# Kernel optimization log

Hardware: AMD Instinct MI355X
Metric: run time of the kernel (lower is better)

## Reference

```python
import jax, jax.numpy as jnp
import numpy as np

# CE module constants (from init_kwargs / chosen input shape)
K = 7        # ksize
S1 = 4       # stride_1 (query patches / fold stride)
S2 = 1       # stride_2 (key/value patches)
SCALE = 10.0 # softmax_scale
C_IN = 32    # in_channels
IC = 4       # inter_channels
B, H, W = 2, 128, 128
PAD1 = ((1, 2), (1, 2))  # 'same' padding for k=7, stride=4, H=W=128 (top=1,bot=2)
PAD2 = ((3, 3), (3, 3))  # 'same' padding for k=7, stride=1


def _conv(x, w, b, stride, pad):
    y = jax.lax.conv_general_dilated(x, w, (stride, stride), pad,
                                     dimension_numbers=('NCHW', 'OIHW', 'NCHW'))
    return y + b[None, :, None, None]


def _patches(x, k, stride, pad):
    # returns [B, L, C*k*k] with feature order (C, kh, kw) == torch.nn.Unfold
    p = jax.lax.conv_general_dilated_patches(x, (k, k), (stride, stride), padding=pad)
    bb, f, ho, wo = p.shape
    return p.reshape(bb, f, ho * wo).transpose(0, 2, 1), ho, wo


def _fold_norm(out, ic, k, hh, ww, stride, pad, lh, lw):
    # out: [B, L1, ic*k*k] -> F.fold(..., (hh,ww), k, padding=pad, stride=stride),
    # normalized by overlap count fold(unfold(ones)).
    bb = out.shape[0]
    z = out.reshape(bb, lh, lw, ic, k, k).transpose(0, 3, 1, 2, 4, 5)  # [B,ic,lh,lw,k,k]
    hp, wp = hh + 2 * pad, ww + 2 * pad
    acc = jnp.zeros((bb, ic, hp, wp), out.dtype)
    cnt = jnp.zeros((hp, wp), out.dtype)
    ih = jnp.arange(lh) * stride
    iw = jnp.arange(lw) * stride
    one = jnp.ones((lh, lw), out.dtype)
    for ki in range(k):
        for kj in range(k):
            r = (ih + ki)[:, None]
            c = (iw + kj)[None, :]
            acc = acc.at[:, :, r, c].add(z[:, :, :, :, ki, kj])
            cnt = cnt.at[r, c].add(one)
    acc = acc[:, :, pad:pad + hh, pad:pad + ww]
    cnt = cnt[pad:pad + hh, pad:pad + ww]
    return acc / cnt


def setup_inputs() -> dict:
    key = jax.random.key(0)
    ks = jax.random.split(key, 13)
    f = K * K * IC  # 196
    g = f // 4      # 49
    s = 0.05
    return {
        'b':       jax.random.normal(ks[0], (B, C_IN, H, W), jnp.float32),
        'w_g':     (jax.random.normal(ks[1], (IC, C_IN, 3, 3), jnp.float32) * s),
        'b_g':     jnp.zeros((IC,), jnp.float32),
        'w_theta': (jax.random.normal(ks[2], (IC, C_IN, 1, 1), jnp.float32) * s),
        'b_theta': jnp.zeros((IC,), jnp.float32),
        'w_fc1':   (jax.random.normal(ks[3], (g, f), jnp.float32) * s),
        'b_fc1':   jnp.zeros((g,), jnp.float32),
        'w_fc2':   (jax.random.normal(ks[4], (g, f), jnp.float32) * s),
        'b_fc2':   jnp.zeros((g,), jnp.float32),
        'w_thr':   (jax.random.normal(ks[5], (1, C_IN, K, K), jnp.float32) * s),
        'b_thr':   jnp.zeros((1,), jnp.float32),
        'w_bias':  (jax.random.normal(ks[6], (1, C_IN, K, K), jnp.float32) * s),
        'b_bias':  jnp.zeros((1,), jnp.float32),
    }


def reference(b, w_g, b_g, w_theta, b_theta, w_fc1, b_fc1, w_fc2, b_fc2,
              w_thr, b_thr, w_bias, b_bias):
    bb = b.shape[0]
    b1 = _conv(b, w_g, b_g, 1, ((1, 1), (1, 1)))        # g: 3x3, pad 1 -> [B,IC,H,W]
    b2 = _conv(b, w_theta, b_theta, 1, ((0, 0), (0, 0)))  # theta: 1x1
    # adaptive threshold / bias per coarse patch (conv on same-padded b)
    thr = _conv(b, w_thr, b_thr, S1, PAD1).reshape(bb, -1)    # [B, L1]
    bias = _conv(b, w_bias, b_bias, S1, PAD1).reshape(bb, -1)  # [B, L1]
    p28, lh, lw = _patches(b1, K, S1, PAD1)   # queries  [B, L1, IC*49]
    p112, _, _ = _patches(b2, K, S2, PAD2)    # values   [B, L2, IC*49]
    p112_2, _, _ = _patches(b1, K, S2, PAD2)  # keys     [B, L2, IC*49] (b3 = b1)
    wi = jax.nn.relu(jnp.einsum('blf,gf->blg', p28, w_fc1) + b_fc1)     # [B,L1,49]
    xi = jax.nn.relu(jnp.einsum('blf,gf->blg', p112_2, w_fc2) + b_fc2)  # [B,L2,49]
    score = jnp.einsum('bpg,bqg->bpq', wi, xi)  # [B, L1, L2]
    mask = jax.nn.relu(score - score.mean(-1, keepdims=True) * thr[:, :, None]
                       + bias[:, :, None])
    mask_b = (mask != 0.0).astype(score.dtype)
    attn = jax.nn.softmax(score * mask * SCALE, axis=-1) * mask_b
    out = jnp.einsum('bpq,bqf->bpf', attn, p112)  # [B, L1, IC*49]
    return _fold_norm(out, IC, K, H, W, S1, 3, lh, lw)  # [B, IC, H, W]
```

## Files before the change

### kernel.cpp

```cpp
#include <hip/hip_runtime.h>
#include <hip/hip_fp16.h>
#include <math.h>

static constexpr int C_IN = 32, IC = 4, H = 128, W = 128, G = 49, F = 196;
static constexpr int L = 1024, Q = 16384;
static constexpr float SCALE = 10.f;
static constexpr int NH = 8;
static constexpr int B2P_PER_B = 8*5*136*136;

typedef __attribute__((ext_vector_type(8))) short short8;
typedef __attribute__((ext_vector_type(4))) float floatx4;

__device__ __forceinline__ unsigned short f2bf(float f){
  unsigned u = __float_as_uint(f);
  return (unsigned short)((u + 0x7fffu + ((u >> 16) & 1u)) >> 16);
}
__device__ __forceinline__ float bf2f(unsigned short h){
  return __uint_as_float(((unsigned)h) << 16);
}
__device__ __forceinline__ floatx4 mfma16(uint4 a, uint4 b, floatx4 c){
  return __builtin_amdgcn_mfma_f32_16x16x32_bf16(*(short8*)&a, *(short8*)&b, c, 0, 0, 0);
}

__global__ __launch_bounds__(256) void k_front(
    const float* __restrict__ bsrc, const float* __restrict__ w_g, const float* __restrict__ b_g,
    const float* __restrict__ w_t, const float* __restrict__ b_t,
    float* __restrict__ b1, unsigned short* __restrict__ b2p) {
  __shared__ float s_wg[IC*C_IN*9];
  __shared__ float s_wt[IC*C_IN];
  __shared__ float s_bg[IC], s_bt[IC];
  for (int i = threadIdx.x; i < IC*C_IN*9; i += 256) s_wg[i] = w_g[i];
  for (int i = threadIdx.x; i < IC*C_IN; i += 256) s_wt[i] = w_t[i];
  if (threadIdx.x < IC) { s_bg[threadIdx.x] = b_g[threadIdx.x]; s_bt[threadIdx.x] = b_t[threadIdx.x]; }
  __syncthreads();
  int idx = blockIdx.x*256 + threadIdx.x;
  int x = idx & 127, y = (idx>>7) & 127, bb = idx >> 14;
  const float* bp = bsrc + (size_t)bb*C_IN*H*W;
  float a1[IC], a2[IC];
  #pragma unroll
  for (int o=0;o<IC;o++){ a1[o]=s_bg[o]; a2[o]=s_bt[o]; }
  for (int c=0;c<C_IN;c++){
    const float* bc = bp + c*H*W;
    float ctr = bc[y*W+x];
    #pragma unroll
    for (int o=0;o<IC;o++) a2[o] += ctr * s_wt[o*C_IN + c];
    #pragma unroll
    for (int dy=0; dy<3; dy++){
      int yy = y + dy - 1;
      if ((unsigned)yy >= (unsigned)H) continue;
      #pragma unroll
      for (int dx=0; dx<3; dx++){
        int xx = x + dx - 1;
        if ((unsigned)xx >= (unsigned)W) continue;
        float v = bc[yy*W+xx];
        #pragma unroll
        for (int o=0;o<IC;o++) a1[o] += v * s_wg[(o*C_IN + c)*9 + dy*3 + dx];
      }
    }
  }
  unsigned short* bp2 = b2p + (size_t)bb*B2P_PER_B;
  #pragma unroll
  for (int o=0;o<IC;o++){
    b1[((size_t)(bb*IC+o)*H + y)*W + x] = a1[o];
    unsigned short h = f2bf(a2[o]);
    #pragma unroll
    for (int s=0;s<7;s++){
      int u = x + 3 - s;
      if (u >= 0)
        bp2[((s*5 + o)*136 + (y+3))*136 + u] = h;
    }
  }
}

__global__ __launch_bounds__(128) void k_xi(
    const float* __restrict__ b1, const float* __restrict__ w_fc2, const float* __restrict__ b_fc2,
    unsigned short* __restrict__ xiT, float* __restrict__ meanxi) {
  __shared__ float s_wT[196][16];
  __shared__ float s_p[IC*7*136];
  __shared__ float s_red[2][16];
  int tid = threadIdx.x;
  int blk = blockIdx.x;
  int gq = blk & 3, y = (blk >> 2) & 127, bb = blk >> 9;
  int g0 = (gq == 0) ? 0 : (13 + 12*(gq-1));
  int ng = (gq == 0) ? 13 : 12;
  for (int i = tid; i < 196*16; i += 128){
    int f = i >> 4, gi = i & 15;
    s_wT[f][gi] = (gi < ng) ? w_fc2[(size_t)(g0+gi)*196 + f] : 0.f;
  }
  for (int i=tid; i<IC*7*136; i+=128) {
    int col = i % 136; int t = i / 136; int ki = t % 7; int c = t / 7;
    int gy = y - 3 + ki, gx = col - 3;
    float v = 0.f;
    if ((unsigned)gy < (unsigned)H && (unsigned)gx < (unsigned)W && col < 134)
      v = b1[((size_t)(bb*IC+c)*H + gy)*W + gx];
    s_p[i] = v;
  }
  __syncthreads();
  int x = tid;
  float acc[13];
  #pragma unroll
  for (int ai=0; ai<13; ++ai) acc[ai] = (ai < ng) ? b_fc2[g0+ai] : 0.f;
  for (int c=0;c<IC;c++)
    for (int ki=0;ki<7;ki++){
      const float* prow = &s_p[(c*7+ki)*136 + x];
      #pragma unroll
      for (int kj=0;kj<7;kj++){
        float pv = prow[kj];
        int f = c*49 + ki*7 + kj;
        const float4* wr = (const float4*)&s_wT[f][0];
        float4 w0 = wr[0], w1 = wr[1], w2 = wr[2], w3 = wr[3];
        float wv[16] = {w0.x,w0.y,w0.z,w0.w, w1.x,w1.y,w1.z,w1.w,
                        w2.x,w2.y,w2.z,w2.w, w3.x,w3.y,w3.z,w3.w};
        #pragma unroll
        for (int ai=0; ai<13; ++ai) acc[ai] += pv * wv[ai];
      }
    }
  #pragma unroll
  for (int ai=0; ai<13; ++ai) acc[ai] = fmaxf(acc[ai], 0.f);
  #pragma unroll
  for (int ai=0; ai<13; ++ai){
    if (ai >= ng) break;
    float v = acc[ai];
    #pragma unroll
    for (int off=1; off<64; off<<=1) v += __shfl_xor(v, off);
    if ((tid&63)==0) s_red[tid>>6][ai] = v;
  }
  __syncthreads();
  if (tid < ng) atomicAdd(&meanxi[bb*G + g0 + tid], (s_red[0][tid]+s_red[1][tid]) * (1.f/(float)Q));
  unsigned short* xr = xiT + ((size_t)((bb<<14) + y*W + x))*128;
  #pragma unroll
  for (int ai=0; ai<13; ++ai){
    if (ai >= ng) break;
    float w = acc[ai];
    unsigned short h = f2bf(w);
    float l = w - bf2f(h);
    xr[g0+ai] = h;
    xr[64+g0+ai] = f2bf(l);
  }
  if (gq == 3){
    for (int gi=49; gi<64; ++gi){ xr[gi] = 0; xr[64+gi] = 0; }
  }
}

__global__ __launch_bounds__(256) void k_wi(
    const float* __restrict__ b1, const float* __restrict__ w_fc1, const float* __restrict__ b_fc1,
    const float* __restrict__ meanxi,
    unsigned short* __restrict__ wiP, float* __restrict__ rowmean) {
  __shared__ float wt[196*52];
  __shared__ float mxs[64];
  int tid = threadIdx.x;
  for (int i=tid; i<G*F; i+=256){ int g = i/F, f = i%F; wt[f*52 + g] = w_fc1[i]; }
  for (int i=tid; i<F*3; i+=256){ int f = i/3; wt[f*52 + 49 + (i%3)] = 0.f; }
  int pg0 = blockIdx.x*4;
  int bb = pg0 >> 10;
  if (tid < 64) mxs[tid] = (tid < G) ? meanxi[bb*G + tid] : 0.f;
  __syncthreads();
  int wave = tid >> 6, g = tid & 63;
  int pg = pg0 + wave;
  int p = pg & 1023;
  int py = p >> 5, px = p & 31;
  float acc = (g < G) ? b_fc1[g] : 0.f;
  for (int c=0;c<IC;c++){
    const float* bc = b1 + (size_t)(bb*IC+c)*H*W;
    for (int ki=0;ki<7;ki++){
      int yy = py*4 - 1 + ki;
      if ((unsigned)yy >= (unsigned)H) continue;
      const float* wrow = &wt[(c*49 + ki*7)*52 + g];
      #pragma unroll
      for (int kj=0;kj<7;kj++){
        int xx = px*4 - 1 + kj;
        if ((unsigned)xx >= (unsigned)W) continue;
        acc += bc[yy*W+xx] * wrow[kj*52];
      }
    }
  }
  acc = fmaxf(acc, 0.f);
  if (g >= G) acc = 0.f;
  float r = acc * mxs[g];
  #pragma unroll
  for (int off=1; off<64; off<<=1) r += __shfl_xor(r, off);
  if (g == 0) rowmean[pg] = r;
  unsigned short h = f2bf(acc);
  float l = acc - bf2f(h);
  size_t base = (size_t)pg*128;
  wiP[base + g] = h;
  wiP[base + 64 + g] = f2bf(l);
}

__global__ __launch_bounds__(256) void k_thrbias(
    const float* __restrict__ bsrc, const float* __restrict__ w_thr, const float* __restrict__ b_thr,
    const float* __restrict__ w_bias, const float* __restrict__ b_bias,
    float* __restrict__ thr, float* __restrict__ bias) {
  int tid = threadIdx.x;
  int c = tid & 31, pl = tid >> 5;
  int pg = blockIdx.x*8 + pl;
  int bb = pg >> 10, p = pg & 1023;
  int py = p >> 5, px = p & 31;
  const float* bc = bsrc + (size_t)(bb*C_IN + c)*H*W;
  float ta = 0.f, ba = 0.f;
  for (int ki=0;ki<7;ki++){
    int yy = py*4 - 1 + ki;
    if ((unsigned)yy >= (unsigned)H) continue;
    #pragma unroll
    for (int kj=0;kj<7;kj++){
      int xx = px*4 - 1 + kj;
      if ((unsigned)xx >= (unsigned)W) continue;
      float v = bc[yy*W+xx];
      ta += v * w_thr[c*49 + ki*7 + kj];
      ba += v * w_bias[c*49 + ki*7 + kj];
    }
  }
  #pragma unroll
  for (int off=1; off<32; off<<=1){ ta += __shfl_xor(ta, off); ba += __shfl_xor(ba, off); }
  if (c == 0) { thr[pg] = ta + b_thr[0]; bias[pg] = ba + b_bias[0]; }
}

__global__ __launch_bounds__(512) void k_attn(
    const unsigned short* __restrict__ b2p, const unsigned short* __restrict__ xiT,
    const unsigned short* __restrict__ wiP, const float* __restrict__ thr,
    const float* __restrict__ bias, const float* __restrict__ rowmean,
    __half* __restrict__ paccT, float* __restrict__ pm, float* __restrict__ pd) {
  __shared__ unsigned short sW[64*280];
  __shared__ float sRed[8][64];
  __shared__ float sM[64];
  int tid = threadIdx.x, lane = tid & 63, wave = tid >> 6;
  int l16 = lane & 15, lg = lane >> 4;
  int wid = blockIdx.x;
  int sp = wid & 7, ptb = (wid >> 3) & 15, bb = wid >> 7;
  int pt2 = wave >> 2, qq = wave & 3;
  int gi0 = (bb<<10) + ptb*64;
  int pl[2] = { pt2*32 + l16, pt2*32 + 16 + l16 };
  float cf[2];
  uint4 wh0[2], wh1[2], wl0[2], wl1[2];
  #pragma unroll
  for (int a=0;a<2;a++){
    int gi = gi0 + pl[a];
    cf[a] = bias[gi] - rowmean[gi]*thr[gi];
    const unsigned short* wr = wiP + (size_t)gi*128;
    wh0[a] = *(const uint4*)&wr[lg*8];
    wh1[a] = *(const uint4*)&wr[32 + lg*8];
    wl0[a] = *(const uint4*)&wr[64 + lg*8];
    wl1[a] = *(const uint4*)&wr[96 + lg*8];
  }
  const unsigned short* xib = xiT + ((size_t)((bb<<14) + sp*2048 + qq*64))*128;
  int bbase = bb * B2P_PER_B;

  float vmax[2] = {0.f, 0.f};
  for (int chunk=0; chunk<8; ++chunk){
    #pragma unroll
    for (int qt=0; qt<4; ++qt){
      const unsigned short* xr = xib + (size_t)(chunk*256 + qt*16 + l16)*128;
      uint4 ah0 = *(const uint4*)&xr[lg*8];
      uint4 ah1 = *(const uint4*)&xr[32 + lg*8];
      uint4 al0 = *(const uint4*)&xr[64 + lg*8];
      uint4 al1 = *(const uint4*)&xr[96 + lg*8];
      #pragma unroll
      for (int a=0;a<2;a++){
        floatx4 s4 = {0.f,0.f,0.f,0.f};
        s4 = mfma16(ah0, wh0[a], s4);
        s4 = mfma16(ah1, wh1[a], s4);
        s4 = mfma16(ah0, wl0[a], s4);
        s4 = mfma16(ah1, wl1[a], s4);
        s4 = mfma16(al0, wh0[a], s4);
        s4 = mfma16(al1, wh1[a], s4);
        #pragma unroll
        for (int j=0;j<4;j++){
          float s = s4[j];
          float v = s * fmaxf(s + cf[a], 0.f) * SCALE;
          vmax[a] = fmaxf(vmax[a], v);
        }
      }
    }
  }
  #pragma unroll
  for (int a=0;a<2;a++){
    vmax[a] = fmaxf(vmax[a], __shfl_xor(vmax[a], 16));
    vmax[a] = fmaxf(vmax[a], __shfl_xor(vmax[a], 32));
    if (lg == 0) sRed[wave][pl[a]] = vmax[a];
  }
  __syncthreads();
  if (tid < 64){
    int p2 = tid >> 5;
    float M = 0.f;
    #pragma unroll
    for (int w=0; w<4; ++w) M = fmaxf(M, sRed[p2*4 + w][tid]);
    sM[tid] = M;
  }
  __syncthreads();
  float Mp[2] = { sM[pl[0]], sM[pl[1]] };
  float dpart[2] = {0.f, 0.f};

  int okf[2]; int At[2]; int fcol[2];
  #pragma unroll
  for (int i=0;i<2;i++){
    int ft = wave + 8*i;
    okf[i] = (ft < 13);
    if (ft > 12) ft = 12;
    int f = ft*16 + l16;
    fcol[i] = f;
    int fc = f/49, rem = f%49, fki = rem/7, fkj = rem%7;
    At[i] = ((fkj*5 + fc)*136 + fki)*136;
  }
  floatx4 acc[2][4];
  #pragma unroll
  for (int i=0;i<2;i++)
    #pragma unroll
    for (int pt=0;pt<4;pt++) acc[i][pt] = (floatx4){0,0,0,0};

  for (int chunk=0; chunk<8; ++chunk){
    #pragma unroll
    for (int qt=0; qt<4; ++qt){
      const unsigned short* xr = xib + (size_t)(chunk*256 + qt*16 + l16)*128;
      uint4 ah0 = *(const uint4*)&xr[lg*8];
      uint4 ah1 = *(const uint4*)&xr[32 + lg*8];
      uint4 al0 = *(const uint4*)&xr[64 + lg*8];
      uint4 al1 = *(const uint4*)&xr[96 + lg*8];
      #pragma unroll
      for (int a=0;a<2;a++){
        floatx4 s4 = {0.f,0.f,0.f,0.f};
        s4 = mfma16(ah0, wh0[a], s4);
        s4 = mfma16(ah1, wh1[a], s4);
        s4 = mfma16(ah0, wl0[a], s4);
        s4 = mfma16(ah1, wl1[a], s4);
        s4 = mfma16(al0, wh0[a], s4);
        s4 = mfma16(al1, wh1[a], s4);
        unsigned pk[2];
        #pragma unroll
        for (int jj=0;jj<2;jj++){
          unsigned lh[2];
          #pragma unroll
          for (int k2=0;k2<2;k2++){
            float s = s4[jj*2+k2];
            float xm = s + cf[a];
            float v = s * fmaxf(xm, 0.f) * SCALE;
            float e = __expf(v - Mp[a]);
            dpart[a] += e;
            lh[k2] = (xm > 0.f) ? (unsigned)f2bf(e) : 0u;
          }
          pk[jj] = lh[0] | (lh[1] << 16);
        }
        uint2 pv = {pk[0], pk[1]};
        *(uint2*)&sW[(size_t)pl[a]*280 + qq*64 + qt*16 + lg*4] = pv;
      }
    }
    __syncthreads();
    int ybase = sp*16 + chunk*2;
    for (int ks=0; ks<8; ++ks){
      int kk = ks*32 + lg*8;
      int y = ybase + (kk >> 7), x8 = kk & 127;
      int gb = bbase + y*136 + x8;
      uint4 bv0 = *(const uint4*)(b2p + gb + At[0]);
      uint4 bv1 = {0,0,0,0};
      if (okf[1]) bv1 = *(const uint4*)(b2p + gb + At[1]);
      #pragma unroll
      for (int pt=0; pt<4; ++pt){
        uint4 a0 = *(const uint4*)&sW[(size_t)(pt*16 + l16)*280 + kk];
        acc[0][pt] = mfma16(a0, bv0, acc[0][pt]);
        if (okf[1]) acc[1][pt] = mfma16(a0, bv1, acc[1][pt]);
      }
    }
    __syncthreads();
  }

  #pragma unroll
  for (int a=0;a<2;a++){
    dpart[a] += __shfl_xor(dpart[a], 16);
    dpart[a] += __shfl_xor(dpart[a], 32);
    if (lg == 0) sRed[wave][pl[a]] = dpart[a];
  }
  __syncthreads();
  int rowbase = ((bb*16 + ptb)*8 + sp)*64;
  if (tid < 64){
    int p2 = tid >> 5;
    float D = 0.f;
    #pragma unroll
    for (int w=0; w<4; ++w) D += sRed[p2*4 + w][tid];
    pm[rowbase + tid] = sM[tid];
    pd[rowbase + tid] = D;
  }
  #pragma unroll
  for (int i=0;i<2;i++){
    if (!okf[i] || fcol[i] >= F) continue;
    #pragma unroll
    for (int pt=0; pt<4; ++pt){
      #pragma unroll
      for (int j=0;j<4;j++){
        int row = rowbase + pt*16 + lg*4 + j;
        paccT[(size_t)fcol[i]*16384 + row] = __float2half(acc[i][pt][j]);
      }
    }
  }
}

__global__ __launch_bounds__(256) void k_combine(
    const __half* __restrict__ paccT, const float* __restrict__ pm, const float* __restrict__ pd,
    float* __restrict__ outpfT){
  int i = blockIdx.x*256 + threadIdx.x;
  if (i >= 2*L*F) return;
  int f = i >> 11;
  int pp = i & 2047;
  int bb = pp >> 10, p = pp & 1023;
  int ptb = p >> 6, r = p & 63;
  int base = ((bb*16 + ptb)*8)*64 + r;
  float M = 0.f;
  #pragma unroll
  for (int hh=0; hh<NH; hh++) M = fmaxf(M, pm[base + hh*64]);
  float num = 0.f, den = 0.f;
  #pragma unroll
  for (int hh=0; hh<NH; hh++){
    float e = __expf(pm[base + hh*64] - M);
    num += e * __half2float(paccT[(size_t)f*16384 + base + hh*64]);
    den += e * pd[base + hh*64];
  }
  outpfT[(size_t)f*2048 + pp] = num/den;
}

__global__ __launch_bounds__(256) void k_fold(const float* __restrict__ outpfT, float* __restrict__ out){
  int i = blockIdx.x*256 + threadIdx.x;
  if (i >= 2*IC*H*W) return;
  int ww = i & 127, hh = (i>>7)&127, c = (i>>14)&3, bb = i>>16;
  int H3 = hh+3, W3 = ww+3;
  int py0 = (H3-3)>>2, py1 = min(31, H3>>2);
  int px0 = (W3-3)>>2, px1 = min(31, W3>>2);
  float s = 0.f; int cnt = 0;
  for (int py=py0; py<=py1; py++){
    int ki = H3 - 4*py;
    for (int px=px0; px<=px1; px++){
      int kj = W3 - 4*px;
      int f = c*49 + ki*7 + kj;
      s += outpfT[(size_t)f*2048 + (bb<<10) + py*32 + px];
      cnt++;
    }
  }
  out[i] = s / (float)cnt;
}

extern "C" void kernel_launch(void* const* d_in, const int* in_sizes, int n_in,
                              void* d_out, int out_size, void* d_ws, size_t ws_size,
                              hipStream_t stream) {
  const float* b      = (const float*)d_in[0];
  const float* w_g    = (const float*)d_in[1];
  const float* b_g    = (const float*)d_in[2];
  const float* w_t    = (const float*)d_in[3];
  const float* b_t    = (const float*)d_in[4];
  const float* w_fc1  = (const float*)d_in[5];
  const float* b_fc1  = (const float*)d_in[6];
  const float* w_fc2  = (const float*)d_in[7];
  const float* b_fc2  = (const float*)d_in[8];
  const float* w_thr  = (const float*)d_in[9];
  const float* b_thr  = (const float*)d_in[10];
  const float* w_bias = (const float*)d_in[11];
  const float* b_bias = (const float*)d_in[12];
  float* out = (float*)d_out;
  float* ws = (float*)d_ws;

  float* b1      = ws;
  unsigned short* b2p = (unsigned short*)(ws + 131072);
  unsigned short* xiT = (unsigned short*)(ws + 870912);
  unsigned short* wiP = (unsigned short*)(ws + 2968064);
  float* meanxi  = ws + 3099136;
  float* thr     = ws + 3099264;
  float* bias    = ws + 3101312;
  float* rowmean = ws + 3103360;
  __half* paccT  = (__half*)(ws + 3105408);
  float* pm      = ws + 4711040;
  float* pd      = ws + 4727424;
  float* outpfT  = ws + 870912;
  (void)in_sizes; (void)n_in; (void)out_size; (void)ws_size;

  hipMemsetAsync(meanxi, 0, 2*G*sizeof(float), stream);
  hipMemsetAsync(b2p, 0, 2*B2P_PER_B*sizeof(unsigned short), stream);
  k_front  <<<128, 256, 0, stream>>>(b, w_g, b_g, w_t, b_t, b1, b2p);
  k_xi     <<<1024, 128, 0, stream>>>(b1, w_fc2, b_fc2, xiT, meanxi);
  k_wi     <<<512, 256, 0, stream>>>(b1, w_fc1, b_fc1, meanxi, wiP, rowmean);
  k_thrbias<<<256, 256, 0, stream>>>(b, w_thr, b_thr, w_bias, b_bias, thr, bias);
  k_attn   <<<256, 512, 0, stream>>>(b2p, xiT, wiP, thr, bias, rowmean, paccT, pm, pd);
  k_combine<<<(2*L*F + 255)/256, 256, 0, stream>>>(paccT, pm, pd, outpfT);
  k_fold   <<<512, 256, 0, stream>>>(outpfT, out);
}
```

Baseline: 238.6 us.

## Fuse two-pass softmax into single-pass online softmax with double-buffered LDS

Replaces the separate max pass and exp/accumulate pass in the attention kernel with an online (flash-style) softmax. Each chunk's scores are computed once and held in registers, and the running max is used to rescale the accumulators and denominator. The P·V MFMA work for the previous chunk is interleaved with score computation for the current chunk using a double-buffered shared-memory tile. This removes the duplicated score MFMAs and xi reloads, at the cost of more registers, an extra LDS buffer, per-chunk rescaling, and two barriers per chunk.

```diff
diff --git a/kernel.cpp b/kernel.cpp
--- a/kernel.cpp
+++ b/kernel.cpp
@@ -220,9 +220,9 @@
     const unsigned short* __restrict__ wiP, const float* __restrict__ thr,
     const float* __restrict__ bias, const float* __restrict__ rowmean,
     __half* __restrict__ paccT, float* __restrict__ pm, float* __restrict__ pd) {
-  __shared__ unsigned short sW[64*280];
+  __shared__ unsigned short sW[2][64*280];
   __shared__ float sRed[8][64];
-  __shared__ float sM[64];
+  __shared__ float sAlpha[64];
   int tid = threadIdx.x, lane = tid & 63, wave = tid >> 6;
   int l16 = lane & 15, lg = lane >> 4;
   int wid = blockIdx.x;
@@ -245,11 +245,42 @@
   const unsigned short* xib = xiT + ((size_t)((bb<<14) + sp*2048 + qq*64))*128;
   int bbase = bb * B2P_PER_B;
 
-  float vmax[2] = {0.f, 0.f};
-  for (int chunk=0; chunk<8; ++chunk){
+  int okf[2]; int At[2]; int fcol[2];
+  #pragma unroll
+  for (int i=0;i<2;i++){
+    int ft = wave + 8*i;
+    okf[i] = (ft < 13);
+    if (ft > 12) ft = 12;
+    int f = ft*16 + l16;
+    fcol[i] = f;
+    int fc = f/49, rem = f%49, fki = rem/7, fkj = rem%7;
+    At[i] = ((fkj*5 + fc)*136 + fki)*136;
+  }
+  floatx4 acc[2][4];
+  #pragma unroll
+  for (int i=0;i<2;i++)
+    #pragma unroll
+    for (int pt=0;pt<4;pt++) acc[i][pt] = (floatx4){0,0,0,0};
+
+  float Mrun[2] = {0.f, 0.f};
+  float dpart[2] = {0.f, 0.f};
+
+  for (int c=0; c<8; ++c){
+    if (c > 0){
+      #pragma unroll
+      for (int pt=0; pt<4; ++pt){
+        float4 av = *(const float4*)&sAlpha[pt*16 + lg*4];
+        floatx4 a4 = {av.x, av.y, av.z, av.w};
+        acc[0][pt] *= a4;
+        acc[1][pt] *= a4;
+      }
+    }
+    float vs[2][16];
+    unsigned mb[2] = {0u, 0u};
+    float vmax[2] = {0.f, 0.f};
     #pragma unroll
     for (int qt=0; qt<4; ++qt){
-      const unsigned short* xr = xib + (size_t)(chunk*256 + qt*16 + l16)*128;
+      const unsigned short* xr = xib + (size_t)(c*256 + qt*16 + l16)*128;
       uint4 ah0 = *(const uint4*)&xr[lg*8];
       uint4 ah1 = *(const uint4*)&xr[32 + lg*8];
       uint4 al0 = *(const uint4*)&xr[64 + lg*8];
@@ -266,85 +297,75 @@
         #pragma unroll
         for (int j=0;j<4;j++){
           float s = s4[j];
-          float v = s * fmaxf(s + cf[a], 0.f) * SCALE;
+          float xm = s + cf[a];
+          if (xm > 0.f) mb[a] |= (1u << (qt*4 + j));
+          float v = s * fmaxf(xm, 0.f) * SCALE;
+          vs[a][qt*4 + j] = v;
           vmax[a] = fmaxf(vmax[a], v);
         }
       }
     }
-  }
-  #pragma unroll
-  for (int a=0;a<2;a++){
-    vmax[a] = fmaxf(vmax[a], __shfl_xor(vmax[a], 16));
-    vmax[a] = fmaxf(vmax[a], __shfl_xor(vmax[a], 32));
-    if (lg == 0) sRed[wave][pl[a]] = vmax[a];
-  }
-  __syncthreads();
-  if (tid < 64){
-    int p2 = tid >> 5;
-    float M = 0.f;
-    #pragma unroll
-    for (int w=0; w<4; ++w) M = fmaxf(M, sRed[p2*4 + w][tid]);
-    sM[tid] = M;
-  }
-  __syncthreads();
-  float Mp[2] = { sM[pl[0]], sM[pl[1]] };
-  float dpart[2] = {0.f, 0.f};
-
-  int okf[2]; int At[2]; int fcol[2];
-  #pragma unroll
-  for (int i=0;i<2;i++){
-    int ft = wave + 8*i;
-    okf[i] = (ft < 13);
-    if (ft > 12) ft = 12;
-    int f = ft*16 + l16;
-    fcol[i] = f;
-    int fc = f/49, rem = f%49, fki = rem/7, fkj = rem%7;
-    At[i] = ((fkj*5 + fc)*136 + fki)*136;
-  }
-  floatx4 acc[2][4];
-  #pragma unroll
-  for (int i=0;i<2;i++)
-    #pragma unroll
-    for (int pt=0;pt<4;pt++) acc[i][pt] = (floatx4){0,0,0,0};
-
-  for (int chunk=0; chunk<8; ++chunk){
-    #pragma unroll
-    for (int qt=0; qt<4; ++qt){
-      const unsigned short* xr = xib + (size_t)(chunk*256 + qt*16 + l16)*128;
-      uint4 ah0 = *(const uint4*)&xr[lg*8];
-      uint4 ah1 = *(const uint4*)&xr[32 + lg*8];
-      uint4 al0 = *(const uint4*)&xr[64 + lg*8];
-      uint4 al1 = *(const uint4*)&xr[96 + lg*8];
-      #pragma unroll
-      for (int a=0;a<2;a++){
-        floatx4 s4 = {0.f,0.f,0.f,0.f};
-        s4 = mfma16(ah0, wh0[a], s4);
-        s4 = mfma16(ah1, wh1[a], s4);
-        s4 = mfma16(ah0, wl0[a], s4);
-        s4 = mfma16(ah1, wl1[a], s4);
-        s4 = mfma16(al0, wh0[a], s4);
-        s4 = mfma16(al1, wh1[a], s4);
-        unsigned pk[2];
+    if (c > 0){
+      int ybase = sp*16 + (c-1)*2;
+      const unsigned short* sWr = &sW[(c-1)&1][0];
+      for (int ks=0; ks<8; ++ks){
+        int kk = ks*32 + lg*8;
+        int y = ybase + (kk >> 7), x8 = kk & 127;
+        int gb = bbase + y*136 + x8;
+        uint4 bv0 = *(const uint4*)(b2p + gb + At[0]);
+        uint4 bv1 = {0,0,0,0};
+        if (okf[1]) bv1 = *(const uint4*)(b2p + gb + At[1]);
         #pragma unroll
-        for (int jj=0;jj<2;jj++){
-          unsigned lh[2];
-          #pragma unroll
-          for (int k2=0;k2<2;k2++){
-            float s = s4[jj*2+k2];
-            float xm = s + cf[a];
-            float v = s * fmaxf(xm, 0.f) * SCALE;
-            float e = __expf(v - Mp[a]);
-            dpart[a] += e;
-            lh[k2] = (xm > 0.f) ? (unsigned)f2bf(e) : 0u;
-          }
-          pk[jj] = lh[0] | (lh[1] << 16);
+        for (int pt=0; pt<4; ++pt){
+          uint4 a0 = *(const uint4*)&sWr[(pt*16 + l16)*280 + kk];
+          acc[0][pt] = mfma16(a0, bv0, acc[0][pt]);
+          if (okf[1]) acc[1][pt] = mfma16(a0, bv1, acc[1][pt]);
         }
-        uint2 pv = {pk[0], pk[1]};
-        *(uint2*)&sW[(size_t)pl[a]*280 + qq*64 + qt*16 + lg*4] = pv;
-      }
+      }
+    }
+    #pragma unroll
+    for (int a=0;a<2;a++){
+      vmax[a] = fmaxf(vmax[a], __shfl_xor(vmax[a], 16));
+      vmax[a] = fmaxf(vmax[a], __shfl_xor(vmax[a], 32));
+      if (lg == 0) sRed[wave][pl[a]] = vmax[a];
     }
     __syncthreads();
-    int ybase = sp*16 + chunk*2;
+    #pragma unroll
+    for (int a=0;a<2;a++){
+      float cm = fmaxf(fmaxf(sRed[pt2*4+0][pl[a]], sRed[pt2*4+1][pl[a]]),
+                       fmaxf(sRed[pt2*4+2][pl[a]], sRed[pt2*4+3][pl[a]]));
+      float Mnew = fmaxf(Mrun[a], cm);
+      float alpha = __expf(Mrun[a] - Mnew);
+      Mrun[a] = Mnew;
+      if (qq == 0 && lg == 0) sAlpha[pl[a]] = alpha;
+      float sum = 0.f;
+      #pragma unroll
+      for (int qt=0; qt<4; ++qt){
+        float e0 = __expf(vs[a][qt*4+0] - Mnew);
+        float e1 = __expf(vs[a][qt*4+1] - Mnew);
+        float e2 = __expf(vs[a][qt*4+2] - Mnew);
+        float e3 = __expf(vs[a][qt*4+3] - Mnew);
+        sum += e0+e1+e2+e3;
+        unsigned m4 = mb[a] >> (qt*4);
+        unsigned w0 = ((m4&1u)? (unsigned)f2bf(e0):0u) | (((m4&2u)? (unsigned)f2bf(e1):0u)<<16);
+        unsigned w1 = ((m4&4u)? (unsigned)f2bf(e2):0u) | (((m4&8u)? (unsigned)f2bf(e3):0u)<<16);
+        uint2 pv = {w0, w1};
+        *(uint2*)&sW[c&1][pl[a]*280 + qq*64 + qt*16 + lg*4] = pv;
+      }
+      dpart[a] = dpart[a]*alpha + sum;
+    }
+    __syncthreads();
+  }
+  #pragma unroll
+  for (int pt=0; pt<4; ++pt){
+    float4 av = *(const float4*)&sAlpha[pt*16 + lg*4];
+    floatx4 a4 = {av.x, av.y, av.z, av.w};
+    acc[0][pt] *= a4;
+    acc[1][pt] *= a4;
+  }
+  {
+    int ybase = sp*16 + 7*2;
+    const unsigned short* sWr = &sW[1][0];
     for (int ks=0; ks<8; ++ks){
       int kk = ks*32 + lg*8;
       int y = ybase + (kk >> 7), x8 = kk & 127;
@@ -354,14 +375,12 @@
       if (okf[1]) bv1 = *(const uint4*)(b2p + gb + At[1]);
       #pragma unroll
       for (int pt=0; pt<4; ++pt){
-        uint4 a0 = *(const uint4*)&sW[(size_t)(pt*16 + l16)*280 + kk];
+        uint4 a0 = *(const uint4*)&sWr[(pt*16 + l16)*280 + kk];
         acc[0][pt] = mfma16(a0, bv0, acc[0][pt]);
         if (okf[1]) acc[1][pt] = mfma16(a0, bv1, acc[1][pt]);
       }
     }
-    __syncthreads();
-  }
-
+  }
   #pragma unroll
   for (int a=0;a<2;a++){
     dpart[a] += __shfl_xor(dpart[a], 16);
@@ -370,13 +389,14 @@
   }
   __syncthreads();
   int rowbase = ((bb*16 + ptb)*8 + sp)*64;
-  if (tid < 64){
-    int p2 = tid >> 5;
-    float D = 0.f;
-    #pragma unroll
-    for (int w=0; w<4; ++w) D += sRed[p2*4 + w][tid];
-    pm[rowbase + tid] = sM[tid];
-    pd[rowbase + tid] = D;
+  if (qq == 0 && lg == 0){
+    #pragma unroll
+    for (int a=0;a<2;a++){
+      float D = sRed[pt2*4+0][pl[a]] + sRed[pt2*4+1][pl[a]]
+              + sRed[pt2*4+2][pl[a]] + sRed[pt2*4+3][pl[a]];
+      pm[rowbase + pl[a]] = Mrun[a];
+      pd[rowbase + pl[a]] = D;
+    }
   }
   #pragma unroll
   for (int i=0;i<2;i++){
```

Measured after the change: 222.9 us. 1.07x faster.
